# Kernel optimization log

Hardware: AMD Instinct MI355X
Metric: run time of the kernel (lower is better)

## Reference

```python
import jax, jax.numpy as jnp
from jax import lax
import numpy as np

B, C, D, H, W = 2, 2, 128, 256, 256
N_PAIRS = 32
N_ITERS = 10
SMOOTH = 1e-5


def setup_inputs() -> dict:
    key = jax.random.key(0)
    k1, k2 = jax.random.split(key)
    logits = jax.random.normal(k1, (B, C, D, H, W), dtype=jnp.float32)
    labels = jax.random.randint(k2, (B, 1, D, H, W), 0, 2).astype(jnp.int32)
    # Replicate the torch module's endpoint sampling (nonzero + randint) with numpy,
    # since it is non-differentiable index bookkeeping, not part of the loss math.
    lab_np = np.asarray(labels)
    rng = np.random.default_rng(0)
    ea = np.zeros((B, N_PAIRS, 3), dtype=np.int32)
    eb = np.zeros((B, N_PAIRS, 3), dtype=np.int32)
    for b in range(B):
        coords = np.argwhere(lab_np[b, 0] > 0)  # (n_fg, 3)
        n_fg = coords.shape[0]
        ia = rng.integers(0, n_fg, size=N_PAIRS)
        ib = rng.integers(0, n_fg, size=N_PAIRS)
        same = ia == ib
        ib[same] = (ib[same] + 1) % n_fg
        ea[b] = coords[ia]
        eb[b] = coords[ib]
    return {
        "logits": logits,
        "labels": labels,
        "endpoints_a": jnp.asarray(ea),
        "endpoints_b": jnp.asarray(eb),
    }


def _avg_pool3d(x):
    # 3x3x3 box filter, stride 1, zero padding, count_include_pad=True (torch default)
    s = lax.reduce_window(x, 0.0, lax.add, (3, 3, 3), (1, 1, 1), "SAME")
    return s / 27.0


def _pair_connectivity(prob, ea, eb):
    # prob: (D,H,W); ea/eb: (n_pairs, 3) int source/target voxel coords
    heat = jnp.zeros_like(prob).at[ea[:, 0], ea[:, 1], ea[:, 2]].set(1.0)

    def step(h, _):
        h = _avg_pool3d(h) * prob
        hmax = h.max()
        h = jnp.where(hmax > 0, h / (hmax + SMOOTH), h)
        return h, None

    heat, _ = lax.scan(step, heat, None, length=N_ITERS)
    scores = heat[eb[:, 0], eb[:, 1], eb[:, 2]]
    return 1.0 - scores.mean()


def reference(logits, labels, endpoints_a, endpoints_b):
    # labels only determined endpoint sampling (done in setup_inputs); loss math uses logits.
    fg_prob = jax.nn.softmax(logits, axis=1)[:, 1]  # (B, D, H, W)
    per_batch = jax.vmap(_pair_connectivity)(fg_prob, endpoints_a, endpoints_b)
    return per_batch.mean()
```

## Files before the change

### kernel.cpp

```cpp
#include <hip/hip_runtime.h>
#include <cstddef>

#define BZ   2
#define DV   128
#define HV   256
#define WV   256
#define NP   32
#define NBOX 64
#define RAD  10
#define BOX  21
#define BOX2 441
#define BOX3 9261
#define HWV  65536
#define DHW  ((size_t)DV*HWV)
#define SMOOTH 1e-5f
#define NT   448

#define ONE_ITER(S, T_, TRK9, TRKN)                                         \
    do {                                                                    \
        if (act) {                                                          \
            _Pragma("unroll")                                               \
            for (int d = 0; d < BOX; ++d) {                                 \
                float lv = (S)[d*BOX2 + tm1];                               \
                float cv = (S)[d*BOX2 + t];                                 \
                float rv = (S)[d*BOX2 + tp1];                               \
                (T_)[d*BOX2 + t] = (wl ? lv : 0.f) + cv + (wr ? rv : 0.f);  \
            }                                                               \
        }                                                                   \
        __syncthreads();                                                    \
        if (act) {                                                          \
            _Pragma("unroll")                                               \
            for (int d = 0; d < BOX; ++d) {                                 \
                float av = (T_)[d*BOX2 + hm1];                              \
                float cv = (T_)[d*BOX2 + t];                                \
                float bv = (T_)[d*BOX2 + hp1];                              \
                (S)[d*BOX2 + t] = (hl ? av : 0.f) + cv + (hr ? bv : 0.f);   \
            }                                                               \
        }                                                                   \
        __syncthreads();                                                    \
        if (act) {                                                          \
            _Pragma("unroll")                                               \
            for (int d = 0; d < BOX; ++d) {                                 \
                float s2 = (S)[d*BOX2 + t];                                 \
                if (d > 0)      s2 += (S)[(d-1)*BOX2 + t];                  \
                if (d < BOX-1)  s2 += (S)[(d+1)*BOX2 + t];                  \
                float v = s2 * p[d];                                        \
                (T_)[d*BOX2 + t] = v;                                       \
                if (TRK9) max9 = fmaxf(max9, v);                            \
                if (TRKN) maxN = fmaxf(maxN, v);                            \
            }                                                               \
        }                                                                   \
        __syncthreads();                                                    \
    } while (0)

__global__ void __launch_bounds__(NT)
evolve_kernel(const float* __restrict__ logits,
              const int* __restrict__ ea,
              float* __restrict__ u,
              float* __restrict__ g9part,
              float* __restrict__ gNpart,
              int* __restrict__ dupflag)
{
    __shared__ float X[BOX3];
    __shared__ float Y[BOX3];
    __shared__ int sE[NBOX][3];
    __shared__ float sred[7], sred2[7];
    __shared__ int sflag;

    const int box = blockIdx.x;
    const int b = box >> 5;
    const int t = threadIdx.x;
    const bool act = (t < BOX2);
    const int hh = t / BOX, ww = t % BOX;

    if (t < NBOX*3) ((int*)sE)[t] = ea[t];
    __syncthreads();
    const int sd = sE[box][0], sh = sE[box][1], sw = sE[box][2];
    if (t < 64) {
        const int pidx = box - b*NP;
        bool pr = false;
        if (t < pidx) {
            int q = b*NP + t;
            pr = (sE[q][0]==sd && sE[q][1]==sh && sE[q][2]==sw);
        }
        unsigned long long m = __ballot(pr);
        if (t == 0) sflag = (m != 0ull);
    }
    __syncthreads();

    if (sflag) {
        if (t == 0) { g9part[box] = 0.f; gNpart[box] = 0.f; dupflag[box] = 1; }
        return;
    }
    if (t == 0) dupflag[box] = 0;

    const bool wl = (ww > 0), wr = (ww < BOX-1);
    const bool hl = (hh > 0), hr = (hh < BOX-1);
    const int tm1 = t + (wl ? -1 : 0);
    const int tp1 = t + (wr ?  1 : 0);
    const int hm1 = t + (hl ? -BOX : 0);
    const int hp1 = t + (hr ?  BOX : 0);

    float p[BOX];
    #pragma unroll
    for (int d = 0; d < BOX; ++d) p[d] = 0.f;
    if (act) {
        const int gh = sh - RAD + hh, gw = sw - RAD + ww;
        if (gh >= 0 && gh < HV && gw >= 0 && gw < WV) {
            const float* lg = logits + (size_t)b * 2 * DHW;
            #pragma unroll
            for (int d = 0; d < BOX; ++d) {
                int gd = sd - RAD + d;
                if (gd >= 0 && gd < DV) {
                    size_t off = (size_t)gd * HWV + (size_t)gh * WV + gw;
                    float l0 = lg[off], l1 = lg[off + DHW];
                    p[d] = (1.f/27.f) / (1.f + __expf(l0 - l1));
                }
            }
        }
    }

    if (act) {
        #pragma unroll
        for (int d = 0; d < BOX; ++d) {
            bool in3 = (d >= RAD-1 && d <= RAD+1) &&
                       (hh >= RAD-1 && hh <= RAD+1) &&
                       (ww >= RAD-1 && ww <= RAD+1);
            X[d*BOX2 + t] = in3 ? p[d] : 0.f;
        }
    }
    __syncthreads();

    float max9 = 0.f, maxN = 0.f;
    for (int kk = 0; kk < 4; ++kk) {
        ONE_ITER(X, Y, false, false);
        ONE_ITER(Y, X, (kk == 3), false);
    }
    ONE_ITER(X, Y, false, true);

    for (int i = t; i < BOX3; i += NT) u[(size_t)box * BOX3 + i] = Y[i];

    #pragma unroll
    for (int o = 32; o > 0; o >>= 1) {
        max9 = fmaxf(max9, __shfl_down(max9, o));
        maxN = fmaxf(maxN, __shfl_down(maxN, o));
    }
    if ((t & 63) == 0) { sred[t >> 6] = max9; sred2[t >> 6] = maxN; }
    __syncthreads();
    if (t == 0) {
        float m9 = sred[0], mN = sred2[0];
        #pragma unroll
        for (int i = 1; i < 7; ++i) { m9 = fmaxf(m9, sred[i]); mN = fmaxf(mN, sred2[i]); }
        g9part[box] = m9;
        gNpart[box] = mN;
    }
}

__global__ void __launch_bounds__(NT)
maxsum_kernel(const int* __restrict__ ea,
              const float* __restrict__ u,
              const int* __restrict__ dupflag,
              float* __restrict__ gNpart)
{
    __shared__ float L[BOX3];
    __shared__ int sE[NBOX][3];
    __shared__ int sdup[NBOX];
    __shared__ int list[NP], ldel[NP][3];
    __shared__ int nlist;
    __shared__ float sred[7];

    const int box = blockIdx.x;
    const int b = box >> 5;
    const int t = threadIdx.x;

    if (t < NBOX*3) ((int*)sE)[t] = ea[t];
    if (t >= NT-NBOX) sdup[t-(NT-NBOX)] = dupflag[t-(NT-NBOX)];
    __syncthreads();
    if (sdup[box]) return;

    if (t == 0) {
        int n = 0;
        const int sd = sE[box][0], sh = sE[box][1], sw = sE[box][2];
        for (int q = b*NP; q < (b+1)*NP; ++q) {
            if (q == box || sdup[q]) continue;
            int dd = sd - sE[q][0], dh = sh - sE[q][1], dw = sw - sE[q][2];
            if (abs(dd) <= 2*RAD && abs(dh) <= 2*RAD && abs(dw) <= 2*RAD) {
                list[n] = q;
                ldel[n][0] = dd; ldel[n][1] = dh; ldel[n][2] = dw;
                ++n;
            }
        }
        nlist = n;
    }
    __syncthreads();
    const int nl = nlist;
    if (nl == 0) return;

    for (int i = t; i < BOX3; i += NT) L[i] = u[(size_t)box * BOX3 + i];
    __syncthreads();

    for (int j = 0; j < nl; ++j) {
        const int dd = ldel[j][0], dh = ldel[j][1], dw = ldel[j][2];
        const int lod = max(0, -dd), hid = min(BOX, BOX - dd);
        const int loh = max(0, -dh), hih = min(BOX, BOX - dh);
        const int low = max(0, -dw), hiw = min(BOX, BOX - dw);
        const int ed = hid - lod, eh = hih - loh, ew = hiw - low;
        const int vol = ed * eh * ew;
        const float* uj = u + (size_t)list[j] * BOX3;
        for (int i = t; i < vol; i += NT) {
            int dl = lod + i / (eh * ew), r = i % (eh * ew);
            int hlq = loh + r / ew, wlq = low + r % ew;
            int own = dl*BOX2 + hlq*BOX + wlq;
            int jid = (dl+dd)*BOX2 + (hlq+dh)*BOX + (wlq+dw);
            L[own] += uj[jid];
        }
        __syncthreads();
    }

    float m = 0.f;
    for (int i = t; i < BOX3; i += NT) m = fmaxf(m, L[i]);
    #pragma unroll
    for (int o = 32; o > 0; o >>= 1) m = fmaxf(m, __shfl_down(m, o));
    if ((t & 63) == 0) sred[t >> 6] = m;
    __syncthreads();
    if (t == 0) {
        float mm = sred[0];
        #pragma unroll
        for (int i = 1; i < 7; ++i) mm = fmaxf(mm, sred[i]);
        gNpart[box] = mm;
    }
}

__global__ void final_kernel(const int* __restrict__ ea,
                             const int* __restrict__ eb,
                             const float* __restrict__ u,
                             const int* __restrict__ dupflag,
                             const float* __restrict__ gNpart,
                             const float* __restrict__ g9part,
                             float* __restrict__ out)
{
    const int t = threadIdx.x;
    const int b = t >> 5;
    float gN = 0.f, g9 = 0.f;
    for (int q = b*NP; q < (b+1)*NP; ++q) {
        gN = fmaxf(gN, gNpart[q]);
        g9 = fmaxf(g9, g9part[q]);
    }
    const float tden = gN + SMOOTH * g9;

    const int d = eb[t*3], h = eb[t*3+1], w = eb[t*3+2];
    float v = 0.f;
    for (int q = b*NP; q < (b+1)*NP; ++q) {
        if (dupflag[q]) continue;
        int ld = d - ea[q*3]   + RAD;
        int lh = h - ea[q*3+1] + RAD;
        int lw = w - ea[q*3+2] + RAD;
        if (ld >= 0 && ld < BOX && lh >= 0 && lh < BOX && lw >= 0 && lw < BOX)
            v += u[(size_t)q * BOX3 + (ld*BOX + lh)*BOX + lw];
    }
    float score = (tden > 0.f) ? v / tden : 0.f;
    #pragma unroll
    for (int o = 32; o > 0; o >>= 1) score += __shfl_down(score, o);
    if (t == 0) out[0] = 1.f - score / (float)NBOX;
}

extern "C" void kernel_launch(void* const* d_in, const int* in_sizes, int n_in,
                              void* d_out, int out_size, void* d_ws, size_t ws_size,
                              hipStream_t stream) {
    const float* logits = (const float*)d_in[0];
    const int* ea = (const int*)d_in[2];
    const int* eb = (const int*)d_in[3];
    float* out = (float*)d_out;

    float* u       = (float*)d_ws;
    float* g9part  = u + (size_t)NBOX * BOX3;
    float* gNpart  = g9part + NBOX;
    int*   dflag   = (int*)(gNpart + NBOX);

    evolve_kernel<<<NBOX, NT, 0, stream>>>(logits, ea, u, g9part, gNpart, dflag);
    maxsum_kernel<<<NBOX, NT, 0, stream>>>(ea, u, dflag, gNpart);
    final_kernel<<<1, 64, 0, stream>>>(ea, eb, u, dflag, gNpart, g9part, out);
}
```

Before: 244.3 us.

## Keep per-thread depth column in registers for box-filter iterations

Restructures the 3D box-filter evolution so each thread holds its full depth column in registers. The depth pass is done in registers, and only the W and H neighbour exchanges go through shared memory, using a column-major layout with stride 21. This removes one shared-memory pass and one barrier per iteration, and writes the output directly from registers. Launch bounds now request two blocks per CU. The risks are higher register pressure and shared-memory bank conflicts from the stride-21 per-thread layout.

```diff
diff --git a/kernel.cpp b/kernel.cpp
--- a/kernel.cpp
+++ b/kernel.cpp
@@ -15,45 +15,9 @@
 #define DHW  ((size_t)DV*HWV)
 #define SMOOTH 1e-5f
 #define NT   448
-
-#define ONE_ITER(S, T_, TRK9, TRKN)                                         \
-    do {                                                                    \
-        if (act) {                                                          \
-            _Pragma("unroll")                                               \
-            for (int d = 0; d < BOX; ++d) {                                 \
-                float lv = (S)[d*BOX2 + tm1];                               \
-                float cv = (S)[d*BOX2 + t];                                 \
-                float rv = (S)[d*BOX2 + tp1];                               \
-                (T_)[d*BOX2 + t] = (wl ? lv : 0.f) + cv + (wr ? rv : 0.f);  \
-            }                                                               \
-        }                                                                   \
-        __syncthreads();                                                    \
-        if (act) {                                                          \
-            _Pragma("unroll")                                               \
-            for (int d = 0; d < BOX; ++d) {                                 \
-                float av = (T_)[d*BOX2 + hm1];                              \
-                float cv = (T_)[d*BOX2 + t];                                \
-                float bv = (T_)[d*BOX2 + hp1];                              \
-                (S)[d*BOX2 + t] = (hl ? av : 0.f) + cv + (hr ? bv : 0.f);   \
-            }                                                               \
-        }                                                                   \
-        __syncthreads();                                                    \
-        if (act) {                                                          \
-            _Pragma("unroll")                                               \
-            for (int d = 0; d < BOX; ++d) {                                 \
-                float s2 = (S)[d*BOX2 + t];                                 \
-                if (d > 0)      s2 += (S)[(d-1)*BOX2 + t];                  \
-                if (d < BOX-1)  s2 += (S)[(d+1)*BOX2 + t];                  \
-                float v = s2 * p[d];                                        \
-                (T_)[d*BOX2 + t] = v;                                       \
-                if (TRK9) max9 = fmaxf(max9, v);                            \
-                if (TRKN) maxN = fmaxf(maxN, v);                            \
-            }                                                               \
-        }                                                                   \
-        __syncthreads();                                                    \
-    } while (0)
-
-__global__ void __launch_bounds__(NT)
+#define CST  21
+
+__global__ void __launch_bounds__(NT, 2)
 evolve_kernel(const float* __restrict__ logits,
               const int* __restrict__ ea,
               float* __restrict__ u,
@@ -61,8 +25,8 @@
               float* __restrict__ gNpart,
               int* __restrict__ dupflag)
 {
-    __shared__ float X[BOX3];
-    __shared__ float Y[BOX3];
+    __shared__ float A[BOX2 * CST];
+    __shared__ float Bb[BOX2 * CST];
     __shared__ int sE[NBOX][3];
     __shared__ float sred[7], sred2[7];
     __shared__ int sflag;
@@ -96,10 +60,6 @@
 
     const bool wl = (ww > 0), wr = (ww < BOX-1);
     const bool hl = (hh > 0), hr = (hh < BOX-1);
-    const int tm1 = t + (wl ? -1 : 0);
-    const int tp1 = t + (wr ?  1 : 0);
-    const int hm1 = t + (hl ? -BOX : 0);
-    const int hp1 = t + (hr ?  BOX : 0);
 
     float p[BOX];
     #pragma unroll
@@ -120,25 +80,71 @@
         }
     }
 
+    float c[BOX];
+    {
+        const bool inhw = (hh >= RAD-1 && hh <= RAD+1) && (ww >= RAD-1 && ww <= RAD+1);
+        #pragma unroll
+        for (int d = 0; d < BOX; ++d)
+            c[d] = (inhw && d >= RAD-1 && d <= RAD+1) ? p[d] : 0.f;
+    }
+
+    float max9 = 0.f, maxN = 0.f;
+    float* const myA = &A[t * CST];
+    float* const myB = &Bb[t * CST];
+
+    for (int k = 0; k < 9; ++k) {
+        float prev = 0.f, cur = c[0];
+        #pragma unroll
+        for (int d = 0; d < BOX; ++d) {
+            float nxt = (d < BOX-1) ? c[d+1] : 0.f;
+            c[d] = prev + cur + nxt;
+            prev = cur; cur = nxt;
+        }
+        if (act) {
+            #pragma unroll
+            for (int d = 0; d < BOX; ++d) myA[d] = c[d];
+        }
+        __syncthreads();
+        if (act) {
+            if (wl) {
+                const float* nb = myA - CST;
+                #pragma unroll
+                for (int d = 0; d < BOX; ++d) c[d] += nb[d];
+            }
+            if (wr) {
+                const float* nb = myA + CST;
+                #pragma unroll
+                for (int d = 0; d < BOX; ++d) c[d] += nb[d];
+            }
+            #pragma unroll
+            for (int d = 0; d < BOX; ++d) myB[d] = c[d];
+        }
+        __syncthreads();
+        if (act) {
+            if (hl) {
+                const float* nb = myB - BOX*CST;
+                #pragma unroll
+                for (int d = 0; d < BOX; ++d) c[d] += nb[d];
+            }
+            if (hr) {
+                const float* nb = myB + BOX*CST;
+                #pragma unroll
+                for (int d = 0; d < BOX; ++d) c[d] += nb[d];
+            }
+        }
+        #pragma unroll
+        for (int d = 0; d < BOX; ++d) {
+            c[d] *= p[d];
+            if (k == 7) max9 = fmaxf(max9, c[d]);
+            if (k == 8) maxN = fmaxf(maxN, c[d]);
+        }
+    }
+
     if (act) {
         #pragma unroll
-        for (int d = 0; d < BOX; ++d) {
-            bool in3 = (d >= RAD-1 && d <= RAD+1) &&
-                       (hh >= RAD-1 && hh <= RAD+1) &&
-                       (ww >= RAD-1 && ww <= RAD+1);
-            X[d*BOX2 + t] = in3 ? p[d] : 0.f;
-        }
-    }
-    __syncthreads();
-
-    float max9 = 0.f, maxN = 0.f;
-    for (int kk = 0; kk < 4; ++kk) {
-        ONE_ITER(X, Y, false, false);
-        ONE_ITER(Y, X, (kk == 3), false);
-    }
-    ONE_ITER(X, Y, false, true);
-
-    for (int i = t; i < BOX3; i += NT) u[(size_t)box * BOX3 + i] = Y[i];
+        for (int d = 0; d < BOX; ++d)
+            u[(size_t)box * BOX3 + d * BOX2 + t] = c[d];
+    }
 
     #pragma unroll
     for (int o = 32; o > 0; o >>= 1) {
```

New measurement: 239.3 us. 1.02x faster.
